# Optimization experiments

Measured on AMD Instinct MI355X. Metric: run time of the kernel, lower is better.

The kernel has to match this reference:

```python
import jax, jax.numpy as jnp
import numpy as np

H = 8
D_MODEL = 512
D_K = 64
D_V = 64
LEN_Q = 1024
LEN_K = 2048
BATCH = 4
EPS = 1e-5


def setup_inputs() -> dict:
    key = jax.random.key(0)
    ks = jax.random.split(key, 12)
    s = 1.0 / np.sqrt(D_MODEL)
    inp = {
        "Q": jax.random.normal(ks[0], (BATCH, LEN_Q, D_MODEL), jnp.float32),
        "K": jax.random.normal(ks[1], (BATCH, LEN_K, D_MODEL), jnp.float32),
        "V": jax.random.normal(ks[2], (BATCH, LEN_K, D_MODEL), jnp.float32),
        "node_num": LEN_K,
        "mask": jax.random.randint(ks[3], (BATCH, LEN_K), 0, 2, jnp.int32),
        "Wq": jax.random.normal(ks[4], (H * D_K, D_MODEL), jnp.float32) * s,
        "bq": jnp.zeros((H * D_K,), jnp.float32),
        "Wk": jax.random.normal(ks[5], (H * D_K, D_MODEL), jnp.float32) * s,
        "bk": jnp.zeros((H * D_K,), jnp.float32),
        "Wv": jax.random.normal(ks[6], (H * D_V, D_MODEL), jnp.float32) * s,
        "bv": jnp.zeros((H * D_V,), jnp.float32),
        "Wo": jax.random.normal(ks[7], (D_MODEL, H * D_V), jnp.float32) * (1.0 / np.sqrt(H * D_V)),
        "bo": jnp.zeros((D_MODEL,), jnp.float32),
        "gamma": jnp.ones((D_MODEL,), jnp.float32),
        "beta": jnp.zeros((D_MODEL,), jnp.float32),
    }
    return inp


def reference(Q, K, V, node_num, mask, Wq, bq, Wk, bk, Wv, bv, Wo, bo, gamma, beta):
    B, Lq, _ = Q.shape
    Lk = K.shape[1]  # node_num
    # QKV projections, split heads: [B, L, H, d]
    q = (jnp.einsum('bqm,em->bqe', Q, Wq) + bq).reshape(B, Lq, H, D_K)
    k = (jnp.einsum('bkm,em->bke', K, Wk) + bk).reshape(B, Lk, H, D_K)
    v = (jnp.einsum('bkm,em->bke', V, Wv) + bv).reshape(B, Lk, H, D_V)
    # scaled dot-product attention with key padding mask
    scores = jnp.einsum('bqhd,bkhd->bhqk', q, k) / jnp.sqrt(jnp.float32(D_K))
    scores = jnp.where(mask[:, None, None, :] == 0, -jnp.inf, scores)
    alpha = jax.nn.softmax(scores, axis=-1)  # [B,H,Lq,Lk]
    out = jnp.einsum('bhqk,bkhd->bqhd', alpha, v).reshape(B, Lq, H * D_V)
    # output projection (dropout is identity in eval) + residual + LayerNorm
    out = jnp.einsum('bqe,me->bqm', out, Wo) + bo + Q
    mu = jnp.mean(out, axis=-1, keepdims=True)
    var = jnp.var(out, axis=-1, keepdims=True)
    out = (out - mu) * jax.lax.rsqrt(var + EPS) * gamma + beta
    return out
```

## Files before the change

kernel.cpp:

```cpp
#include <hip/hip_runtime.h>
#include <math.h>

#define H 8
#define DM 512
#define DK 64
#define LQ 1024
#define LK 2048
#define BATCH 4
#define LN_EPS 1e-5f

typedef short s16x8 __attribute__((ext_vector_type(8)));
typedef float f32x16 __attribute__((ext_vector_type(16)));

union U32x4 { unsigned u[4]; s16x8 v; };

__device__ __forceinline__ unsigned f2bf_rne(unsigned u) {
    return (u + 0x7fffu + ((u >> 16) & 1u)) >> 16;
}
__device__ __forceinline__ void cvt_split(float x, short& h, short& l) {
    unsigned u = __float_as_uint(x);
    unsigned hb = f2bf_rne(u);
    float hf = __uint_as_float(hb << 16);
    unsigned lb = f2bf_rne(__float_as_uint(x - hf));
    h = (short)hb; l = (short)lb;
}
__device__ __forceinline__ unsigned pack_bf16(float a, float b) {
    return f2bf_rne(__float_as_uint(a)) | (f2bf_rne(__float_as_uint(b)) << 16);
}

#define LDP 40

template <int MODE>
__device__ __forceinline__ void gemm_mfma_body(short* __restrict__ Ah,
                                               short* __restrict__ Al,
                                               short* __restrict__ Bh,
                                               short* __restrict__ Bl,
                                               const float* __restrict__ A,
                                               const float* __restrict__ W,
                                               const float* __restrict__ bias,
                                               const float* __restrict__ resid,
                                               float* __restrict__ C,
                                               short* __restrict__ dsth,
                                               short* __restrict__ dstl,
                                               long m0, int n0)
{
    const int tid = threadIdx.x;
    const int l   = tid & 63;
    const int w   = tid >> 6;
    const int wm  = w >> 1, wn = w & 1;

    f32x16 acc[2][2];
#pragma unroll
    for (int mi = 0; mi < 2; ++mi)
#pragma unroll
        for (int ni = 0; ni < 2; ++ni)
#pragma unroll
            for (int e = 0; e < 16; ++e) acc[mi][ni][e] = 0.f;

    const int srow = tid >> 1;
    const int skb  = (tid & 1) * 16;

    for (int k0 = 0; k0 < DM; k0 += 32) {
        __syncthreads();
        {
            const float* src = A + (m0 + srow) * DM + k0 + skb;
            float fa[16];
            *(float4*)&fa[0]  = *(const float4*)(src + 0);
            *(float4*)&fa[4]  = *(const float4*)(src + 4);
            *(float4*)&fa[8]  = *(const float4*)(src + 8);
            *(float4*)&fa[12] = *(const float4*)(src + 12);
            s16x8 vh0, vl0, vh1, vl1;
#pragma unroll
            for (int j = 0; j < 8; ++j) { short hh, ll; cvt_split(fa[j], hh, ll); vh0[j] = hh; vl0[j] = ll; }
#pragma unroll
            for (int j = 0; j < 8; ++j) { short hh, ll; cvt_split(fa[8 + j], hh, ll); vh1[j] = hh; vl1[j] = ll; }
            *(s16x8*)&Ah[srow * LDP + skb]     = vh0;
            *(s16x8*)&Ah[srow * LDP + skb + 8] = vh1;
            *(s16x8*)&Al[srow * LDP + skb]     = vl0;
            *(s16x8*)&Al[srow * LDP + skb + 8] = vl1;
        }
        {
            const float* src = W + (long)(n0 + srow) * DM + k0 + skb;
            float fb[16];
            *(float4*)&fb[0]  = *(const float4*)(src + 0);
            *(float4*)&fb[4]  = *(const float4*)(src + 4);
            *(float4*)&fb[8]  = *(const float4*)(src + 8);
            *(float4*)&fb[12] = *(const float4*)(src + 12);
            s16x8 vh0, vl0, vh1, vl1;
#pragma unroll
            for (int j = 0; j < 8; ++j) { short hh, ll; cvt_split(fb[j], hh, ll); vh0[j] = hh; vl0[j] = ll; }
#pragma unroll
            for (int j = 0; j < 8; ++j) { short hh, ll; cvt_split(fb[8 + j], hh, ll); vh1[j] = hh; vl1[j] = ll; }
            *(s16x8*)&Bh[srow * LDP + skb]     = vh0;
            *(s16x8*)&Bh[srow * LDP + skb + 8] = vh1;
            *(s16x8*)&Bl[srow * LDP + skb]     = vl0;
            *(s16x8*)&Bl[srow * LDP + skb + 8] = vl1;
        }
        __syncthreads();

#pragma unroll
        for (int kk = 0; kk < 32; kk += 16) {
            const int ko = kk + (l >> 5) * 8;
            s16x8 ah[2], al2[2], bh[2], bl[2];
#pragma unroll
            for (int mi = 0; mi < 2; ++mi) {
                int r = wm * 64 + mi * 32 + (l & 31);
                ah[mi]  = *(const s16x8*)&Ah[r * LDP + ko];
                al2[mi] = *(const s16x8*)&Al[r * LDP + ko];
            }
#pragma unroll
            for (int ni = 0; ni < 2; ++ni) {
                int r = wn * 64 + ni * 32 + (l & 31);
                bh[ni] = *(const s16x8*)&Bh[r * LDP + ko];
                bl[ni] = *(const s16x8*)&Bl[r * LDP + ko];
            }
#pragma unroll
            for (int mi = 0; mi < 2; ++mi)
#pragma unroll
                for (int ni = 0; ni < 2; ++ni) {
                    acc[mi][ni] = __builtin_amdgcn_mfma_f32_32x32x16_bf16(ah[mi],  bh[ni], acc[mi][ni], 0, 0, 0);
                    acc[mi][ni] = __builtin_amdgcn_mfma_f32_32x32x16_bf16(ah[mi],  bl[ni], acc[mi][ni], 0, 0, 0);
                    acc[mi][ni] = __builtin_amdgcn_mfma_f32_32x32x16_bf16(al2[mi], bh[ni], acc[mi][ni], 0, 0, 0);
                }
        }
    }

#pragma unroll
    for (int mi = 0; mi < 2; ++mi)
#pragma unroll
        for (int ni = 0; ni < 2; ++ni) {
            const int n = n0 + wn * 64 + ni * 32 + (l & 31);
            const float bv = bias[n];
            const long mbase = m0 + wm * 64 + mi * 32 + 4 * (l >> 5);
#pragma unroll
            for (int reg = 0; reg < 16; ++reg) {
                long m = mbase + (reg & 3) + 8 * (reg >> 2);
                float val = acc[mi][ni][reg] + bv;
                if (MODE == 0) {
                    if (resid) val += resid[m * DM + n];
                    C[m * DM + n] = val;
                } else {
                    short hv, lv; cvt_split(val, hv, lv);
                    int b2 = (int)(m >> 11), key = (int)(m & 2047);
                    int h2 = n >> 6, d = n & 63;
                    if (MODE == 1) {
                        long idx = ((long)(b2 * 8 + h2) * 2048 + key) * 64 + d;
                        dsth[idx] = hv; dstl[idx] = lv;
                    } else {
                        long idx = ((long)(b2 * 8 + h2) * 64 + d) * 2048 + key;
                        dsth[idx] = hv; dstl[idx] = lv;
                    }
                }
            }
        }
}

__global__ __launch_bounds__(256, 4) void qkv_kernel(const float* __restrict__ Q,
                                                     const float* __restrict__ K,
                                                     const float* __restrict__ V,
                                                     const float* __restrict__ Wq,
                                                     const float* __restrict__ bq,
                                                     const float* __restrict__ Wk,
                                                     const float* __restrict__ bk,
                                                     const float* __restrict__ Wv,
                                                     const float* __restrict__ bv,
                                                     float* __restrict__ qp,
                                                     short* __restrict__ kbh,
                                                     short* __restrict__ kbl,
                                                     short* __restrict__ vth,
                                                     short* __restrict__ vtl)
{
    __shared__ __align__(16) short Ah[128 * LDP];
    __shared__ __align__(16) short Al[128 * LDP];
    __shared__ __align__(16) short Bh[128 * LDP];
    __shared__ __align__(16) short Bl[128 * LDP];

    const int bx = blockIdx.x;
    if (bx < 128) {
        gemm_mfma_body<0>(Ah, Al, Bh, Bl, Q, Wq, bq, nullptr, qp, nullptr, nullptr,
                          (long)(bx >> 2) * 128, (bx & 3) * 128);
    } else if (bx < 384) {
        int t = bx - 128;
        gemm_mfma_body<1>(Ah, Al, Bh, Bl, K, Wk, bk, nullptr, nullptr, kbh, kbl,
                          (long)(t >> 2) * 128, (t & 3) * 128);
    } else {
        int t = bx - 384;
        gemm_mfma_body<2>(Ah, Al, Bh, Bl, V, Wv, bv, nullptr, nullptr, vth, vtl,
                          (long)(t >> 2) * 128, (t & 3) * 128);
    }
}

__global__ __launch_bounds__(256, 4) void ogemm_kernel(const float* __restrict__ A,
                                                       const float* __restrict__ W,
                                                       const float* __restrict__ bias,
                                                       const float* __restrict__ resid,
                                                       float* __restrict__ C)
{
    __shared__ __align__(16) short Ah[128 * LDP];
    __shared__ __align__(16) short Al[128 * LDP];
    __shared__ __align__(16) short Bh[128 * LDP];
    __shared__ __align__(16) short Bl[128 * LDP];

    const int bx = blockIdx.x;
    gemm_mfma_body<0>(Ah, Al, Bh, Bl, A, W, bias, resid, C, nullptr, nullptr,
                      (long)(bx >> 2) * 128, (bx & 3) * 128);
}

__global__ __launch_bounds__(256, 2) void attn_kernel(const float* __restrict__ qp,
                                                      const short* __restrict__ kbh,
                                                      const short* __restrict__ kbl,
                                                      const short* __restrict__ vth,
                                                      const short* __restrict__ vtl,
                                                      const int* __restrict__ mask,
                                                      float* __restrict__ o)
{
    __shared__ float Obuf[4][64][68];
    __shared__ float mlbuf[4][4][32];

    const int tid = threadIdx.x;
    const int l   = tid & 63;
    const int w   = tid >> 6;
    const int lq  = l & 31;
    const int hi  = l >> 5;

    const int wg  = (blockIdx.x & 7) * 64 + (blockIdx.x >> 3);
    const int q0  = (wg & 15) * 64;
    const int bh  = wg >> 4;
    const int b   = bh >> 3, h = bh & 7;

    s16x8 Qh[2][4], Ql[2][4];
#pragma unroll
    for (int nq = 0; nq < 2; ++nq)
#pragma unroll
        for (int ks = 0; ks < 4; ++ks) {
            const float* src = qp + ((long)(b * LQ + q0 + nq * 32 + lq)) * DM + h * DK + ks * 16 + hi * 8;
            float4 f0 = *(const float4*)src;
            float4 f1 = *(const float4*)(src + 4);
            float ff[8] = {f0.x, f0.y, f0.z, f0.w, f1.x, f1.y, f1.z, f1.w};
            U32x4 Hh, Ll;
#pragma unroll
            for (int i = 0; i < 4; ++i) {
                short h0, l0, h1, l1;
                cvt_split(ff[2 * i] * 0.125f, h0, l0);
                cvt_split(ff[2 * i + 1] * 0.125f, h1, l1);
                Hh.u[i] = (unsigned short)h0 | ((unsigned)(unsigned short)h1 << 16);
                Ll.u[i] = (unsigned short)l0 | ((unsigned)(unsigned short)l1 << 16);
            }
            Qh[nq][ks] = Hh.v; Ql[nq][ks] = Ll.v;
        }

    const short* kbase_h = kbh + (long)bh * 2048 * 64;
    const short* kbase_l = kbl + (long)bh * 2048 * 64;
    const short* vbase_h = vth + (long)bh * 64 * 2048;
    const short* vbase_l = vtl + (long)bh * 64 * 2048;
    const int*   mrow    = mask + b * LK;

    float m_run[2] = {-1e30f, -1e30f};
    float l_run[2] = {0.f, 0.f};
    f32x16 Oa[2][2];
#pragma unroll
    for (int md = 0; md < 2; ++md)
#pragma unroll
        for (int nq = 0; nq < 2; ++nq)
#pragma unroll
            for (int e = 0; e < 16; ++e) Oa[md][nq][e] = 0.f;

    for (int t = 0; t < 16; ++t) {
        const int kt = t * 128 + w * 32;
        const unsigned long long mb = __ballot(mrow[kt + lq] != 0);
        const unsigned mbits = (unsigned)mb;

        f32x16 S[2];
#pragma unroll
        for (int nq = 0; nq < 2; ++nq)
#pragma unroll
            for (int e = 0; e < 16; ++e) S[nq][e] = 0.f;
#pragma unroll
        for (int ks = 0; ks < 4; ++ks) {
            s16x8 Kh = *(const s16x8*)(kbase_h + (long)(kt + lq) * 64 + ks * 16 + hi * 8);
            s16x8 Kl = *(const s16x8*)(kbase_l + (long)(kt + lq) * 64 + ks * 16 + hi * 8);
#pragma unroll
            for (int nq = 0; nq < 2; ++nq) {
                S[nq] = __builtin_amdgcn_mfma_f32_32x32x16_bf16(Kh, Qh[nq][ks], S[nq], 0, 0, 0);
                S[nq] = __builtin_amdgcn_mfma_f32_32x32x16_bf16(Kh, Ql[nq][ks], S[nq], 0, 0, 0);
                S[nq] = __builtin_amdgcn_mfma_f32_32x32x16_bf16(Kl, Qh[nq][ks], S[nq], 0, 0, 0);
            }
        }

        unsigned pk_[2][8], xk[2][8];
#pragma unroll
        for (int nq = 0; nq < 2; ++nq) {
            float sv[16];
#pragma unroll
            for (int r = 0; r < 16; ++r) {
                int key = (r & 3) + 8 * (r >> 2) + 4 * hi;
                sv[r] = ((mbits >> key) & 1u) ? S[nq][r] : -1e30f;
            }
            float mx = sv[0];
#pragma unroll
            for (int r = 1; r < 16; ++r) mx = fmaxf(mx, sv[r]);
            mx = fmaxf(mx, __shfl_xor(mx, 32));
            float m_new = fmaxf(m_run[nq], mx);
            float al = __expf(m_run[nq] - m_new);
            m_run[nq] = m_new;
            float pv[16], ps = 0.f;
#pragma unroll
            for (int r = 0; r < 16; ++r) {
                int key = (r & 3) + 8 * (r >> 2) + 4 * hi;
                float p = ((mbits >> key) & 1u) ? __expf(sv[r] - m_new) : 0.f;
                pv[r] = p; ps += p;
            }
            ps += __shfl_xor(ps, 32);
            l_run[nq] = l_run[nq] * al + ps;
#pragma unroll
            for (int md = 0; md < 2; ++md)
#pragma unroll
                for (int e = 0; e < 16; ++e) Oa[md][nq][e] *= al;
#pragma unroll
            for (int i = 0; i < 8; ++i) pk_[nq][i] = pack_bf16(pv[2 * i], pv[2 * i + 1]);
#pragma unroll
            for (int i = 0; i < 8; ++i) xk[nq][i] = (unsigned)__shfl_xor((int)pk_[nq][i], 32);
        }

#pragma unroll
        for (int ks = 0; ks < 2; ++ks) {
            s16x8 Pf[2];
#pragma unroll
            for (int nq = 0; nq < 2; ++nq) {
                U32x4 u;
                if (hi == 0) {
                    u.u[0] = pk_[nq][4 * ks];     u.u[1] = pk_[nq][4 * ks + 1];
                    u.u[2] = xk[nq][4 * ks];      u.u[3] = xk[nq][4 * ks + 1];
                } else {
                    u.u[0] = xk[nq][4 * ks + 2];  u.u[1] = xk[nq][4 * ks + 3];
                    u.u[2] = pk_[nq][4 * ks + 2]; u.u[3] = pk_[nq][4 * ks + 3];
                }
                Pf[nq] = u.v;
            }
#pragma unroll
            for (int md = 0; md < 2; ++md) {
                s16x8 Vh = *(const s16x8*)(vbase_h + (long)(32 * md + lq) * 2048 + kt + ks * 16 + hi * 8);
                s16x8 Vl = *(const s16x8*)(vbase_l + (long)(32 * md + lq) * 2048 + kt + ks * 16 + hi * 8);
#pragma unroll
                for (int nq = 0; nq < 2; ++nq) {
                    Oa[md][nq] = __builtin_amdgcn_mfma_f32_32x32x16_bf16(Vh, Pf[nq], Oa[md][nq], 0, 0, 0);
                    Oa[md][nq] = __builtin_amdgcn_mfma_f32_32x32x16_bf16(Vl, Pf[nq], Oa[md][nq], 0, 0, 0);
                }
            }
        }
    }

#pragma unroll
    for (int md = 0; md < 2; ++md)
#pragma unroll
        for (int nq = 0; nq < 2; ++nq)
#pragma unroll
            for (int r = 0; r < 16; ++r) {
                int d = 32 * md + (r & 3) + 8 * (r >> 2) + 4 * hi;
                Obuf[w][d][nq * 32 + lq] = Oa[md][nq][r];
            }
    if (l < 32) {
        mlbuf[w][0][lq] = m_run[0];
        mlbuf[w][1][lq] = m_run[1];
        mlbuf[w][2][lq] = l_run[0];
        mlbuf[w][3][lq] = l_run[1];
    }
    __syncthreads();

    {
        const int q  = tid & 63;
        const int dc = tid >> 6;
        const int qh = q >> 5, qlo = q & 31;
        float mw[4], lw[4];
#pragma unroll
        for (int w2 = 0; w2 < 4; ++w2) {
            mw[w2] = mlbuf[w2][qh][qlo];
            lw[w2] = mlbuf[w2][2 + qh][qlo];
        }
        float ms = fmaxf(fmaxf(mw[0], mw[1]), fmaxf(mw[2], mw[3]));
        float fw[4], Ls = 0.f;
#pragma unroll
        for (int w2 = 0; w2 < 4; ++w2) { fw[w2] = __expf(mw[w2] - ms); Ls += lw[w2] * fw[w2]; }
        float inv = 1.f / Ls;
        float ov[16];
#pragma unroll
        for (int dd = 0; dd < 16; ++dd) {
            int d = dc * 16 + dd;
            float a = Obuf[0][d][q] * fw[0] + Obuf[1][d][q] * fw[1] +
                      Obuf[2][d][q] * fw[2] + Obuf[3][d][q] * fw[3];
            ov[dd] = a * inv;
        }
        float* dst = o + ((long)(b * LQ + q0 + q)) * DM + h * DK + dc * 16;
        *(float4*)(dst + 0)  = *(float4*)&ov[0];
        *(float4*)(dst + 4)  = *(float4*)&ov[4];
        *(float4*)(dst + 8)  = *(float4*)&ov[8];
        *(float4*)(dst + 12) = *(float4*)&ov[12];
    }
}

__global__ __launch_bounds__(256) void ln_kernel(const float* __restrict__ x,
                                                 const float* __restrict__ gamma,
                                                 const float* __restrict__ beta,
                                                 float* __restrict__ out)
{
    const int wave = threadIdx.x >> 6;
    const int lane = threadIdx.x & 63;
    const long row = (long)blockIdx.x * 4 + wave;
    const float* xr = x + row * DM + lane * 8;
    float4 a = *(const float4*)xr;
    float4 b = *(const float4*)(xr + 4);
    float sum = a.x + a.y + a.z + a.w + b.x + b.y + b.z + b.w;
    float sq  = a.x * a.x + a.y * a.y + a.z * a.z + a.w * a.w +
                b.x * b.x + b.y * b.y + b.z * b.z + b.w * b.w;
#pragma unroll
    for (int m = 1; m < 64; m <<= 1) {
        sum += __shfl_xor(sum, m);
        sq  += __shfl_xor(sq, m);
    }
    const float mu  = sum * (1.f / 512.f);
    const float var = sq * (1.f / 512.f) - mu * mu;
    const float rs  = 1.0f / sqrtf(var + LN_EPS);

    float4 g0 = *(const float4*)(gamma + lane * 8);
    float4 g1 = *(const float4*)(gamma + lane * 8 + 4);
    float4 t0 = *(const float4*)(beta + lane * 8);
    float4 t1 = *(const float4*)(beta + lane * 8 + 4);
    float4 o0 = make_float4((a.x - mu) * rs * g0.x + t0.x,
                            (a.y - mu) * rs * g0.y + t0.y,
                            (a.z - mu) * rs * g0.z + t0.z,
                            (a.w - mu) * rs * g0.w + t0.w);
    float4 o1 = make_float4((b.x - mu) * rs * g1.x + t1.x,
                            (b.y - mu) * rs * g1.y + t1.y,
                            (b.z - mu) * rs * g1.z + t1.z,
                            (b.w - mu) * rs * g1.w + t1.w);
    *(float4*)(out + row * DM + lane * 8) = o0;
    *(float4*)(out + row * DM + lane * 8 + 4) = o1;
}

extern "C" void kernel_launch(void* const* d_in, const int* in_sizes, int n_in,
                              void* d_out, int out_size, void* d_ws, size_t ws_size,
                              hipStream_t stream)
{
    const float* Q    = (const float*)d_in[0];
    const float* K    = (const float*)d_in[1];
    const float* V    = (const float*)d_in[2];
    const int*   mask = (const int*)d_in[4];
    const float* Wq   = (const float*)d_in[5];
    const float* bq   = (const float*)d_in[6];
    const float* Wk   = (const float*)d_in[7];
    const float* bk   = (const float*)d_in[8];
    const float* Wv   = (const float*)d_in[9];
    const float* bv   = (const float*)d_in[10];
    const float* Wo   = (const float*)d_in[11];
    const float* bo   = (const float*)d_in[12];
    const float* gamma= (const float*)d_in[13];
    const float* beta = (const float*)d_in[14];
    float* out = (float*)d_out;

    char* base = (char*)d_ws;
    float* qp  = (float*)(base);
    short* kbh = (short*)(base + (size_t)8  * 1024 * 1024);
    short* kbl = (short*)(base + (size_t)16 * 1024 * 1024);
    short* vth = (short*)(base + (size_t)24 * 1024 * 1024);
    short* vtl = (short*)(base + (size_t)32 * 1024 * 1024);
    float* ao  = (float*)(base + (size_t)40 * 1024 * 1024);
    float* tmp = (float*)(base + (size_t)48 * 1024 * 1024);

    qkv_kernel<<<640, 256, 0, stream>>>(Q, K, V, Wq, bq, Wk, bk, Wv, bv,
                                        qp, kbh, kbl, vth, vtl);
    attn_kernel<<<512, 256, 0, stream>>>(qp, kbh, kbl, vth, vtl, mask, ao);
    ogemm_kernel<<<128, 256, 0, stream>>>(ao, Wo, bo, Q, tmp);
    ln_kernel<<<1024, 256, 0, stream>>>(tmp, gamma, beta, out);
}
```

Baseline: 296.7 us.

## Halve attention query tile to 32 rows, doubling blocks and occupancy

```diff
diff --git a/kernel.cpp b/kernel.cpp
--- a/kernel.cpp
+++ b/kernel.cpp
@@ -206,7 +206,7 @@
                       (long)(bx >> 2) * 128, (bx & 3) * 128);
 }
 
-__global__ __launch_bounds__(256, 2) void attn_kernel(const float* __restrict__ qp,
+__global__ __launch_bounds__(256, 4) void attn_kernel(const float* __restrict__ qp,
                                                       const short* __restrict__ kbh,
                                                       const short* __restrict__ kbl,
                                                       const short* __restrict__ vth,
@@ -214,8 +214,8 @@
                                                       const int* __restrict__ mask,
                                                       float* __restrict__ o)
 {
-    __shared__ float Obuf[4][64][68];
-    __shared__ float mlbuf[4][4][32];
+    __shared__ float Obuf[4][64][36];
+    __shared__ float mlbuf[4][2][32];
 
     const int tid = threadIdx.x;
     const int l   = tid & 63;
@@ -223,31 +223,29 @@
     const int lq  = l & 31;
     const int hi  = l >> 5;
 
-    const int wg  = (blockIdx.x & 7) * 64 + (blockIdx.x >> 3);
-    const int q0  = (wg & 15) * 64;
-    const int bh  = wg >> 4;
+    const int wg  = (blockIdx.x & 7) * 128 + (blockIdx.x >> 3);
+    const int q0  = (wg & 31) * 32;
+    const int bh  = wg >> 5;
     const int b   = bh >> 3, h = bh & 7;
 
-    s16x8 Qh[2][4], Ql[2][4];
-#pragma unroll
-    for (int nq = 0; nq < 2; ++nq)
-#pragma unroll
-        for (int ks = 0; ks < 4; ++ks) {
-            const float* src = qp + ((long)(b * LQ + q0 + nq * 32 + lq)) * DM + h * DK + ks * 16 + hi * 8;
-            float4 f0 = *(const float4*)src;
-            float4 f1 = *(const float4*)(src + 4);
-            float ff[8] = {f0.x, f0.y, f0.z, f0.w, f1.x, f1.y, f1.z, f1.w};
-            U32x4 Hh, Ll;
-#pragma unroll
-            for (int i = 0; i < 4; ++i) {
-                short h0, l0, h1, l1;
-                cvt_split(ff[2 * i] * 0.125f, h0, l0);
-                cvt_split(ff[2 * i + 1] * 0.125f, h1, l1);
-                Hh.u[i] = (unsigned short)h0 | ((unsigned)(unsigned short)h1 << 16);
-                Ll.u[i] = (unsigned short)l0 | ((unsigned)(unsigned short)l1 << 16);
-            }
-            Qh[nq][ks] = Hh.v; Ql[nq][ks] = Ll.v;
-        }
+    s16x8 Qh[4], Ql[4];
+#pragma unroll
+    for (int ks = 0; ks < 4; ++ks) {
+        const float* src = qp + ((long)(b * LQ + q0 + lq)) * DM + h * DK + ks * 16 + hi * 8;
+        float4 f0 = *(const float4*)src;
+        float4 f1 = *(const float4*)(src + 4);
+        float ff[8] = {f0.x, f0.y, f0.z, f0.w, f1.x, f1.y, f1.z, f1.w};
+        U32x4 Hh, Ll;
+#pragma unroll
+        for (int i = 0; i < 4; ++i) {
+            short h0, l0, h1, l1;
+            cvt_split(ff[2 * i] * 0.125f, h0, l0);
+            cvt_split(ff[2 * i + 1] * 0.125f, h1, l1);
+            Hh.u[i] = (unsigned short)h0 | ((unsigned)(unsigned short)h1 << 16);
+            Ll.u[i] = (unsigned short)l0 | ((unsigned)(unsigned short)l1 << 16);
+        }
+        Qh[ks] = Hh.v; Ql[ks] = Ll.v;
+    }
 
     const short* kbase_h = kbh + (long)bh * 2048 * 64;
     const short* kbase_l = kbl + (long)bh * 2048 * 64;
@@ -255,97 +253,80 @@
     const short* vbase_l = vtl + (long)bh * 64 * 2048;
     const int*   mrow    = mask + b * LK;
 
-    float m_run[2] = {-1e30f, -1e30f};
-    float l_run[2] = {0.f, 0.f};
-    f32x16 Oa[2][2];
+    float m_run = -1e30f;
+    float l_run = 0.f;
+    f32x16 Oa[2];
 #pragma unroll
     for (int md = 0; md < 2; ++md)
 #pragma unroll
-        for (int nq = 0; nq < 2; ++nq)
-#pragma unroll
-            for (int e = 0; e < 16; ++e) Oa[md][nq][e] = 0.f;
+        for (int e = 0; e < 16; ++e) Oa[md][e] = 0.f;
 
     for (int t = 0; t < 16; ++t) {
         const int kt = t * 128 + w * 32;
         const unsigned long long mb = __ballot(mrow[kt + lq] != 0);
         const unsigned mbits = (unsigned)mb;
 
-        f32x16 S[2];
-#pragma unroll
-        for (int nq = 0; nq < 2; ++nq)
-#pragma unroll
-            for (int e = 0; e < 16; ++e) S[nq][e] = 0.f;
+        f32x16 S;
+#pragma unroll
+        for (int e = 0; e < 16; ++e) S[e] = 0.f;
 #pragma unroll
         for (int ks = 0; ks < 4; ++ks) {
             s16x8 Kh = *(const s16x8*)(kbase_h + (long)(kt + lq) * 64 + ks * 16 + hi * 8);
             s16x8 Kl = *(const s16x8*)(kbase_l + (long)(kt + lq) * 64 + ks * 16 + hi * 8);
-#pragma unroll
-            for (int nq = 0; nq < 2; ++nq) {
-                S[nq] = __builtin_amdgcn_mfma_f32_32x32x16_bf16(Kh, Qh[nq][ks], S[nq], 0, 0, 0);
-                S[nq] = __builtin_amdgcn_mfma_f32_32x32x16_bf16(Kh, Ql[nq][ks], S[nq], 0, 0, 0);
-                S[nq] = __builtin_amdgcn_mfma_f32_32x32x16_bf16(Kl, Qh[nq][ks], S[nq], 0, 0, 0);
+            S = __builtin_amdgcn_mfma_f32_32x32x16_bf16(Kh, Qh[ks], S, 0, 0, 0);
+            S = __builtin_amdgcn_mfma_f32_32x32x16_bf16(Kh, Ql[ks], S, 0, 0, 0);
+            S = __builtin_amdgcn_mfma_f32_32x32x16_bf16(Kl, Qh[ks], S, 0, 0, 0);
+        }
+
+        float sv[16];
+#pragma unroll
+        for (int r = 0; r < 16; ++r) {
+            int key = (r & 3) + 8 * (r >> 2) + 4 * hi;
+            sv[r] = ((mbits >> key) & 1u) ? S[r] : -1e30f;
+        }
+        float mx = sv[0];
+#pragma unroll
+        for (int r = 1; r < 16; ++r) mx = fmaxf(mx, sv[r]);
+        mx = fmaxf(mx, __shfl_xor(mx, 32));
+        float m_new = fmaxf(m_run, mx);
+        float al = __expf(m_run - m_new);
+        m_run = m_new;
+        float pv[16], ps = 0.f;
+#pragma unroll
+        for (int r = 0; r < 16; ++r) {
+            int key = (r & 3) + 8 * (r >> 2) + 4 * hi;
+            float p = ((mbits >> key) & 1u) ? __expf(sv[r] - m_new) : 0.f;
+            pv[r] = p; ps += p;
+        }
+        ps += __shfl_xor(ps, 32);
+        l_run = l_run * al + ps;
+#pragma unroll
+        for (int md = 0; md < 2; ++md)
+#pragma unroll
+            for (int e = 0; e < 16; ++e) Oa[md][e] *= al;
+        unsigned pk_[8], xk[8];
+#pragma unroll
+        for (int i = 0; i < 8; ++i) pk_[i] = pack_bf16(pv[2 * i], pv[2 * i + 1]);
+#pragma unroll
+        for (int i = 0; i < 8; ++i) xk[i] = (unsigned)__shfl_xor((int)pk_[i], 32);
+
+#pragma unroll
+        for (int ks = 0; ks < 2; ++ks) {
+            U32x4 u;
+            if (hi == 0) {
+                u.u[0] = pk_[4 * ks];     u.u[1] = pk_[4 * ks + 1];
+                u.u[2] = xk[4 * ks];      u.u[3] = xk[4 * ks + 1];
+            } else {
+                u.u[0] = xk[4 * ks + 2];  u.u[1] = xk[4 * ks + 3];
+                u.u[2] = pk_[4 * ks + 2]; u.u[3] = pk_[4 * ks + 3];
             }
-        }
-
-        unsigned pk_[2][8], xk[2][8];
-#pragma unroll
-        for (int nq = 0; nq < 2; ++nq) {
-            float sv[16];
-#pragma unroll
-            for (int r = 0; r < 16; ++r) {
-                int key = (r & 3) + 8 * (r >> 2) + 4 * hi;
-                sv[r] = ((mbits >> key) & 1u) ? S[nq][r] : -1e30f;
-            }
-            float mx = sv[0];
-#pragma unroll
-            for (int r = 1; r < 16; ++r) mx = fmaxf(mx, sv[r]);
-            mx = fmaxf(mx, __shfl_xor(mx, 32));
-            float m_new = fmaxf(m_run[nq], mx);
-            float al = __expf(m_run[nq] - m_new);
-            m_run[nq] = m_new;
-            float pv[16], ps = 0.f;
-#pragma unroll
-            for (int r = 0; r < 16; ++r) {
-                int key = (r & 3) + 8 * (r >> 2) + 4 * hi;
-                float p = ((mbits >> key) & 1u) ? __expf(sv[r] - m_new) : 0.f;
-                pv[r] = p; ps += p;
-            }
-            ps += __shfl_xor(ps, 32);
-            l_run[nq] = l_run[nq] * al + ps;
-#pragma unroll
-            for (int md = 0; md < 2; ++md)
-#pragma unroll
-                for (int e = 0; e < 16; ++e) Oa[md][nq][e] *= al;
-#pragma unroll
-            for (int i = 0; i < 8; ++i) pk_[nq][i] = pack_bf16(pv[2 * i], pv[2 * i + 1]);
-#pragma unroll
-            for (int i = 0; i < 8; ++i) xk[nq][i] = (unsigned)__shfl_xor((int)pk_[nq][i], 32);
-        }
-
-#pragma unroll
-        for (int ks = 0; ks < 2; ++ks) {
-            s16x8 Pf[2];
-#pragma unroll
-            for (int nq = 0; nq < 2; ++nq) {
-                U32x4 u;
-                if (hi == 0) {
-                    u.u[0] = pk_[nq][4 * ks];     u.u[1] = pk_[nq][4 * ks + 1];
-                    u.u[2] = xk[nq][4 * ks];      u.u[3] = xk[nq][4 * ks + 1];
-                } else {
-                    u.u[0] = xk[nq][4 * ks + 2];  u.u[1] = xk[nq][4 * ks + 3];
-                    u.u[2] = pk_[nq][4 * ks + 2]; u.u[3] = pk_[nq][4 * ks + 3];
-                }
-                Pf[nq] = u.v;
-            }
+            s16x8 Pf = u.v;
 #pragma unroll
             for (int md = 0; md < 2; ++md) {
                 s16x8 Vh = *(const s16x8*)(vbase_h + (long)(32 * md + lq) * 2048 + kt + ks * 16 + hi * 8);
                 s16x8 Vl = *(const s16x8*)(vbase_l + (long)(32 * md + lq) * 2048 + kt + ks * 16 + hi * 8);
-#pragma unroll
-                for (int nq = 0; nq < 2; ++nq) {
-                    Oa[md][nq] = __builtin_amdgcn_mfma_f32_32x32x16_bf16(Vh, Pf[nq], Oa[md][nq], 0, 0, 0);
-                    Oa[md][nq] = __builtin_amdgcn_mfma_f32_32x32x16_bf16(Vl, Pf[nq], Oa[md][nq], 0, 0, 0);
-                }
+                Oa[md] = __builtin_amdgcn_mfma_f32_32x32x16_bf16(Vh, Pf, Oa[md], 0, 0, 0);
+                Oa[md] = __builtin_amdgcn_mfma_f32_32x32x16_bf16(Vl, Pf, Oa[md], 0, 0, 0);
             }
         }
     }
@@ -353,48 +334,41 @@
 #pragma unroll
     for (int md = 0; md < 2; ++md)
 #pragma unroll
-        for (int nq = 0; nq < 2; ++nq)
-#pragma unroll
-            for (int r = 0; r < 16; ++r) {
-                int d = 32 * md + (r & 3) + 8 * (r >> 2) + 4 * hi;
-                Obuf[w][d][nq * 32 + lq] = Oa[md][nq][r];
-            }
+        for (int r = 0; r < 16; ++r) {
+            int d = 32 * md + (r & 3) + 8 * (r >> 2) + 4 * hi;
+            Obuf[w][d][lq] = Oa[md][r];
+        }
     if (l < 32) {
-        mlbuf[w][0][lq] = m_run[0];
-        mlbuf[w][1][lq] = m_run[1];
-        mlbuf[w][2][lq] = l_run[0];
-        mlbuf[w][3][lq] = l_run[1];
+        mlbuf[w][0][lq] = m_run;
+        mlbuf[w][1][lq] = l_run;
     }
     __syncthreads();
 
     {
-        const int q  = tid & 63;
-        const int dc = tid >> 6;
-        const int qh = q >> 5, qlo = q & 31;
+        const int q  = tid & 31;
+        const int dc = tid >> 5;
         float mw[4], lw[4];
 #pragma unroll
         for (int w2 = 0; w2 < 4; ++w2) {
-            mw[w2] = mlbuf[w2][qh][qlo];
-            lw[w2] = mlbuf[w2][2 + qh][qlo];
+            mw[w2] = mlbuf[w2][0][q];
+            lw[w2] = mlbuf[w2][1][q];
         }
         float ms = fmaxf(fmaxf(mw[0], mw[1]), fmaxf(mw[2], mw[3]));
         float fw[4], Ls = 0.f;
 #pragma unroll
         for (int w2 = 0; w2 < 4; ++w2) { fw[w2] = __expf(mw[w2] - ms); Ls += lw[w2] * fw[w2]; }
         float inv = 1.f / Ls;
-        float ov[16];
-#pragma unroll
-        for (int dd = 0; dd < 16; ++dd) {
-            int d = dc * 16 + dd;
+        float ov[8];
+#pragma unroll
+        for (int dd = 0; dd < 8; ++dd) {
+            int d = dc * 8 + dd;
             float a = Obuf[0][d][q] * fw[0] + Obuf[1][d][q] * fw[1] +
                       Obuf[2][d][q] * fw[2] + Obuf[3][d][q] * fw[3];
             ov[dd] = a * inv;
         }
-        float* dst = o + ((long)(b * LQ + q0 + q)) * DM + h * DK + dc * 16;
-        *(float4*)(dst + 0)  = *(float4*)&ov[0];
-        *(float4*)(dst + 4)  = *(float4*)&ov[4];
-        *(float4*)(dst + 8)  = *(float4*)&ov[8];
-        *(float4*)(dst + 12) = *(float4*)&ov[12];
+        float* dst = o + ((long)(b * LQ + q0 + q)) * DM + h * DK + dc * 8;
+        *(float4*)(dst + 0) = *(float4*)&ov[0];
+        *(float4*)(dst + 4) = *(float4*)&ov[4];
     }
 }
 
@@ -468,7 +442,7 @@
 
     qkv_kernel<<<640, 256, 0, stream>>>(Q, K, V, Wq, bq, Wk, bk, Wv, bv,
                                         qp, kbh, kbl, vth, vtl);
-    attn_kernel<<<512, 256, 0, stream>>>(qp, kbh, kbl, vth, vtl, mask, ao);
+    attn_kernel<<<1024, 256, 0, stream>>>(qp, kbh, kbl, vth, vtl, mask, ao);
     ogemm_kernel<<<128, 256, 0, stream>>>(ao, Wo, bo, Q, tmp);
     ln_kernel<<<1024, 256, 0, stream>>>(tmp, gamma, beta, out);
 }
```

After: 361.3 us. 1.22x slower.
